# Optimization experiments

Measured on AMD Instinct MI355X. Metric: run time of the kernel, lower is better.

Reference implementation:

```python
import jax, jax.numpy as jnp
import numpy as np

PADDED = 128  # params.get_padded_size()


def setup_inputs() -> dict:
    key = jax.random.key(0)
    k1, k2 = jax.random.split(key)
    B, N, C = 128, 64, 16  # batch, patch size, gridsize**2 channels
    patches = jax.random.normal(k1, (B, N, N, C), dtype=jnp.float32)
    # fractional pixel offsets; keep patches inside the padded canvas
    positions = jax.random.uniform(k2, (B, C, 2), dtype=jnp.float32,
                                   minval=-20.0, maxval=20.0)
    return {"patches": patches, "positions": positions}


def reference(patches, positions):
    """Reassemble overlapping patches into a padded canvas.

    patches:   [B, N, N, C] real patch stack (C = gridsize**2)
    positions: [B, C, 2] per-patch (dy, dx) pixel offsets
    returns:   [B, PADDED, PADDED, 1] sum of translated patches
    """
    B, N, _, C = patches.shape
    M = PADDED
    pad = (M - N) // 2
    # channel -> flat: [B*C, N, N]
    flat = jnp.transpose(patches, (0, 3, 1, 2)).reshape(B * C, N, N)
    # center-pad each patch to the full canvas: [B*C, M, M]
    padded = jnp.pad(flat, ((0, 0), (pad, M - N - pad), (pad, M - N - pad)))
    # Fourier-shift translate by per-patch subpixel offsets
    off = positions.reshape(B * C, 2)
    dy = off[:, 0][:, None, None]
    dx = off[:, 1][:, None, None]
    f = jnp.fft.fftfreq(M).astype(jnp.float32)
    phase = jnp.exp((-2j * jnp.pi) * (f[None, :, None] * dy + f[None, None, :] * dx)).astype(jnp.complex64)
    shifted = jnp.real(jnp.fft.ifft2(jnp.fft.fft2(padded) * phase))
    # flat -> channel, then accumulate (scatter-add) across the C patches
    out = shifted.reshape(B, C, M, M).sum(axis=1)[..., None]
    return out
```

## Files before the change

kernel.cpp:

```cpp
#include <hip/hip_runtime.h>


#define NCH 16
#define CG  4
#define WPB 4

typedef __attribute__((ext_vector_type(8))) short bf16x8;
typedef __attribute__((ext_vector_type(4))) float f32x4;

__device__ __forceinline__ ushort f2bf(float x) {
    union { float f; uint u; } v; v.f = x;
    uint r = v.u + 0x7fffu + ((v.u >> 16) & 1u);
    return (ushort)(r >> 16);
}
__device__ __forceinline__ float bf2f(ushort h) {
    union { uint u; float f; } v; v.u = ((uint)h) << 16; return v.f;
}
__device__ __forceinline__ int uSw(int x) { return (x ^ (x >> 3)) & 7; }

template<bool USE_WS>
__global__ __launch_bounds__(256, 2)
void reassemble_mfma(const float* __restrict__ patches,
                     const float* __restrict__ positions,
                     float* __restrict__ dst, int B)
{
    __shared__ __align__(16) ushort sTab[2][2][8][200];
    __shared__ __align__(16) ushort sP[2][4096];
    __shared__ __align__(16) ushort sU[2][8192];
    __shared__ float sQ[4];

    const int tid  = threadIdx.x;
    const int lane = tid & 63;
    const int wv   = tid >> 6;
    const int nn   = lane & 15;
    const int hh   = lane >> 4;

    int b, cg;
    if (B == 128) {
        const int xcd = blockIdx.x & 7, slot = blockIdx.x >> 3;
        b = xcd * 16 + (slot >> 2); cg = slot & 3;
    } else { b = blockIdx.x >> 2; cg = blockIdx.x & 3; }

    const f32x4 zero = {0.f, 0.f, 0.f, 0.f};
    f32x4 acc[2][8];
    #pragma unroll
    for (int i = 0; i < 2; ++i)
        #pragma unroll
        for (int j = 0; j < 8; ++j) acc[i][j] = zero;
    float Stot = 0.f;

    const float PI = 3.14159265358979323846f;

    for (int cc = 0; cc < CG; ++cc) {
        const int c = cg * CG + cc;
        __syncthreads();

        const float dy = positions[(b * NCH + c) * 2 + 0];
        const float dx = positions[(b * NCH + c) * 2 + 1];
        float kdxf = rintf(dx), kdyf = rintf(dy);
        float sx = sinf((dx - kdxf) * PI); if (((int)kdxf) & 1) sx = -sx;
        float sy = sinf((dy - kdyf) * PI); if (((int)kdyf) & 1) sy = -sy;

        for (int job = tid; job < 384; job += 256) {
            const int tbl = (job >= 192) ? 1 : 0;
            const int j   = job - 192 * tbl;
            const float d  = tbl ? dy : dx;
            const float sd = tbl ? sy : sx;
            const int t = 223 - j;
            float u   = (float)t - d;
            float ur  = u - 128.f * rintf(u * (1.f / 128.f));
            float th  = ur * (PI / 128.f);
            float sth = sinf(th), cth = cosf(th);
            float v = (fabsf(sth) < 1e-12f) ? ((t & 1) ? 128.f : -128.f)
                                            : sd * cth / sth;
            const ushort hi = f2bf(v);
            const ushort lo = f2bf(v - bf2f(hi));
            #pragma unroll
            for (int a = 0; a < 8; ++a) {
                sTab[tbl][0][a][j + a] = hi;
                sTab[tbl][1][a][j + a] = lo;
            }
        }

        float qp = 0.f;
        {
            const float* src = patches + (size_t)b * 65536 + c;
            const int m0 = 2 * (lane & 31);
            const int rb = lane >> 5;
            #pragma unroll
            for (int pp = 0; pp < 8; ++pp) {
                const int r = 16 * wv + 2 * pp + rb;
                const float v0 = src[(size_t)(r * 64 + m0) * 16];
                const float v1 = src[(size_t)(r * 64 + m0 + 1) * 16];
                const int odd = (r + m0) & 1;
                const float s0 = odd ? -v0 : v0;
                const float s1 = odd ? v1 : -v1;
                qp += s0 + s1;
                const ushort h0 = f2bf(s0), h1 = f2bf(s1);
                const ushort l0 = f2bf(s0 - bf2f(h0)), l1 = f2bf(s1 - bf2f(h1));
                const int idx = r * 64 + (((m0 >> 3) ^ (r & 7)) << 3) + (m0 & 7);
                *(uint*)&sP[0][idx] = (uint)h0 | ((uint)h1 << 16);
                *(uint*)&sP[1][idx] = (uint)l0 | ((uint)l1 << 16);
            }
        }
        #pragma unroll
        for (int off = 32; off >= 1; off >>= 1) qp += __shfl_down(qp, off, 64);
        if (lane == 0) sQ[wv] = qp;

        __syncthreads();

        Stot += sx * sy * (sQ[0] + sQ[1] + sQ[2] + sQ[3]);

        f32x4 accA[8];
        #pragma unroll
        for (int tx = 0; tx < 8; ++tx) accA[tx] = zero;

        #pragma unroll
        for (int ks = 0; ks < 2; ++ks) {
            const int r  = 16 * wv + nn;
            const int mc = 4 * ks + hh;
            const bf16x8 Ah = *(const bf16x8*)&sP[0][r * 64 + ((mc ^ (r & 7)) << 3)];
            const bf16x8 Al = *(const bf16x8*)&sP[1][r * 64 + ((mc ^ (r & 7)) << 3)];
            #pragma unroll
            for (int tx = 0; tx < 8; ++tx) {
                const int e0 = 16 * tx + nn + 96 - 32 * ks - 8 * hh;
                const int j0 = 223 - e0;
                const int a  = (-j0) & 7;
                const bf16x8 Bh = *(const bf16x8*)&sTab[0][0][a][j0 + a];
                const bf16x8 Bl = *(const bf16x8*)&sTab[0][1][a][j0 + a];
                accA[tx] = __builtin_amdgcn_mfma_f32_16x16x32_bf16(Ah, Bh, accA[tx], 0, 0, 0);
                accA[tx] = __builtin_amdgcn_mfma_f32_16x16x32_bf16(Ah, Bl, accA[tx], 0, 0, 0);
                accA[tx] = __builtin_amdgcn_mfma_f32_16x16x32_bf16(Al, Bh, accA[tx], 0, 0, 0);
            }
        }

        #pragma unroll
        for (int tx = 0; tx < 8; ++tx) {
            const int x  = 16 * tx + nn;
            const int r0 = 16 * wv + 4 * hh;
            #pragma unroll
            for (int p = 0; p < 2; ++p) {
                const float v0 = accA[tx][2 * p], v1 = accA[tx][2 * p + 1];
                const ushort h0 = f2bf(v0), h1 = f2bf(v1);
                const ushort l0 = f2bf(v0 - bf2f(h0)), l1 = f2bf(v1 - bf2f(h1));
                const int rr  = r0 + 2 * p;
                const int idx = x * 64 + ((((rr >> 3) ^ uSw(x))) << 3) + (rr & 7);
                *(uint*)&sU[0][idx] = (uint)h0 | ((uint)h1 << 16);
                *(uint*)&sU[1][idx] = (uint)l0 | ((uint)l1 << 16);
            }
        }

        __syncthreads();

        #pragma unroll
        for (int ks = 0; ks < 2; ++ks) {
            #pragma unroll
            for (int sp = 0; sp < 3; ++sp) {
                const int sa = (sp == 2) ? 1 : 0;
                const int sb = (sp == 1) ? 1 : 0;
                bf16x8 A0, A1;
                {
                    const int e0 = 16 * (2 * wv + 0) + nn + 96 - 32 * ks - 8 * hh;
                    const int j0 = 223 - e0, a = (-j0) & 7;
                    A0 = *(const bf16x8*)&sTab[1][sa][a][j0 + a];
                }
                {
                    const int e0 = 16 * (2 * wv + 1) + nn + 96 - 32 * ks - 8 * hh;
                    const int j0 = 223 - e0, a = (-j0) & 7;
                    A1 = *(const bf16x8*)&sTab[1][sa][a][j0 + a];
                }
                const int rc = 4 * ks + hh;
                #pragma unroll
                for (int tx = 0; tx < 8; ++tx) {
                    const int x = 16 * tx + nn;
                    const bf16x8 Bu = *(const bf16x8*)&sU[sb][x * 64 + ((rc ^ uSw(x)) << 3)];
                    acc[0][tx] = __builtin_amdgcn_mfma_f32_16x16x32_bf16(A0, Bu, acc[0][tx], 0, 0, 0);
                    acc[1][tx] = __builtin_amdgcn_mfma_f32_16x16x32_bf16(A1, Bu, acc[1][tx], 0, 0, 0);
                }
            }
        }
    }

    const float inv = 1.f / 16384.f;
    if (USE_WS) {
        float* pb = dst + (size_t)(b * WPB + cg) * 16384;
        #pragma unroll
        for (int tyl = 0; tyl < 2; ++tyl)
            #pragma unroll
            for (int g = 0; g < 4; ++g) {
                const int y = 16 * (2 * wv + tyl) + 4 * hh + g;
                #pragma unroll
                for (int tx = 0; tx < 8; ++tx) {
                    const int x = 16 * tx + nn;
                    const float v = (acc[tyl][tx][g] - Stot) * inv;
                    pb[y * 128 + x] = ((x + y) & 1) ? -v : v;
                }
            }
    } else {
        float* ob = dst + (size_t)b * 16384;
        #pragma unroll
        for (int tyl = 0; tyl < 2; ++tyl)
            #pragma unroll
            for (int g = 0; g < 4; ++g) {
                const int y = 16 * (2 * wv + tyl) + 4 * hh + g;
                #pragma unroll
                for (int tx = 0; tx < 8; ++tx) {
                    const int x = 16 * tx + nn;
                    const float v = (acc[tyl][tx][g] - Stot) * inv;
                    atomicAdd(&ob[y * 128 + x], ((x + y) & 1) ? -v : v);
                }
            }
    }
}

__global__ __launch_bounds__(256)
void reduce_kernel(const float* __restrict__ ws, float* __restrict__ out, int B)
{
    const int t4 = blockIdx.x * 256 + threadIdx.x;
    if (t4 >= B * 4096) return;
    const int b = t4 >> 12, q = t4 & 4095;
    const f32x4* w4 = (const f32x4*)ws;
    f32x4 s = w4[(size_t)(b * WPB) * 4096 + q];
    #pragma unroll
    for (int g = 1; g < WPB; ++g) {
        f32x4 v = w4[(size_t)(b * WPB + g) * 4096 + q];
        s[0] += v[0]; s[1] += v[1]; s[2] += v[2]; s[3] += v[3];
    }
    ((f32x4*)out)[t4] = s;
}

extern "C" void kernel_launch(void* const* d_in, const int* in_sizes, int n_in,
                              void* d_out, int out_size, void* d_ws, size_t ws_size,
                              hipStream_t stream)
{
    const float* patches   = (const float*)d_in[0];
    const float* positions = (const float*)d_in[1];
    float* out = (float*)d_out;

    const int B = in_sizes[1] / (NCH * 2);
    const size_t need = (size_t)B * WPB * 16384 * sizeof(float);

    if (ws_size >= need) {
        reassemble_mfma<true><<<dim3(B * 4), dim3(256), 0, stream>>>(
            patches, positions, (float*)d_ws, B);
        reduce_kernel<<<dim3((B * 4096 + 255) / 256), dim3(256), 0, stream>>>(
            (const float*)d_ws, out, B);
    } else {
        hipMemsetAsync(d_out, 0, (size_t)out_size * sizeof(float), stream);
        reassemble_mfma<false><<<dim3(B * 4), dim3(256), 0, stream>>>(
            patches, positions, out, B);
    }
}
```

Measured before the change: 110.1 us.

## Split channels across more blocks and load patch fragments directly into registers

Halves the channels per block (CG 4→2) so the grid doubles to B*8 blocks, with a larger workspace and more partial sums for the reduce kernel. Patch data now goes straight from global memory into MFMA A-fragment registers, which removes the sP shared buffer and one round trip through LDS. The sU stores are widened to 8-byte vector writes, the second-stage loop is reordered to share loads, and the occupancy hint is raised to 3 blocks per CU. The extra workspace traffic in the reduce step and the uncoalesced strided per-lane global loads could offset these savings.

```diff
diff --git a/kernel.cpp b/kernel.cpp
--- a/kernel.cpp
+++ b/kernel.cpp
@@ -2,11 +2,12 @@
 
 
 #define NCH 16
-#define CG  4
-#define WPB 4
+#define CG  2
+#define WPB 8
 
 typedef __attribute__((ext_vector_type(8))) short bf16x8;
 typedef __attribute__((ext_vector_type(4))) float f32x4;
+typedef __attribute__((ext_vector_type(2))) uint uint2v;
 
 __device__ __forceinline__ ushort f2bf(float x) {
     union { float f; uint u; } v; v.f = x;
@@ -19,13 +20,12 @@
 __device__ __forceinline__ int uSw(int x) { return (x ^ (x >> 3)) & 7; }
 
 template<bool USE_WS>
-__global__ __launch_bounds__(256, 2)
+__global__ __launch_bounds__(256, 3)
 void reassemble_mfma(const float* __restrict__ patches,
                      const float* __restrict__ positions,
                      float* __restrict__ dst, int B)
 {
     __shared__ __align__(16) ushort sTab[2][2][8][200];
-    __shared__ __align__(16) ushort sP[2][4096];
     __shared__ __align__(16) ushort sU[2][8192];
     __shared__ float sQ[4];
 
@@ -38,8 +38,8 @@
     int b, cg;
     if (B == 128) {
         const int xcd = blockIdx.x & 7, slot = blockIdx.x >> 3;
-        b = xcd * 16 + (slot >> 2); cg = slot & 3;
-    } else { b = blockIdx.x >> 2; cg = blockIdx.x & 3; }
+        b = xcd * 16 + (slot >> 3); cg = slot & 7;
+    } else { b = blockIdx.x >> 3; cg = blockIdx.x & 7; }
 
     const f32x4 zero = {0.f, 0.f, 0.f, 0.f};
     f32x4 acc[2][8];
@@ -82,25 +82,24 @@
             }
         }
 
+        bf16x8 Ah[2], Al[2];
         float qp = 0.f;
         {
             const float* src = patches + (size_t)b * 65536 + c;
-            const int m0 = 2 * (lane & 31);
-            const int rb = lane >> 5;
-            #pragma unroll
-            for (int pp = 0; pp < 8; ++pp) {
-                const int r = 16 * wv + 2 * pp + rb;
-                const float v0 = src[(size_t)(r * 64 + m0) * 16];
-                const float v1 = src[(size_t)(r * 64 + m0 + 1) * 16];
-                const int odd = (r + m0) & 1;
-                const float s0 = odd ? -v0 : v0;
-                const float s1 = odd ? v1 : -v1;
-                qp += s0 + s1;
-                const ushort h0 = f2bf(s0), h1 = f2bf(s1);
-                const ushort l0 = f2bf(s0 - bf2f(h0)), l1 = f2bf(s1 - bf2f(h1));
-                const int idx = r * 64 + (((m0 >> 3) ^ (r & 7)) << 3) + (m0 & 7);
-                *(uint*)&sP[0][idx] = (uint)h0 | ((uint)h1 << 16);
-                *(uint*)&sP[1][idx] = (uint)l0 | ((uint)l1 << 16);
+            const int r = 16 * wv + nn;
+            #pragma unroll
+            for (int ks = 0; ks < 2; ++ks) {
+                #pragma unroll
+                for (int d8 = 0; d8 < 8; ++d8) {
+                    const int m = 32 * ks + 8 * hh + d8;
+                    const float v  = src[(size_t)(r * 64 + m) * 16];
+                    const float sv = ((r + m) & 1) ? -v : v;
+                    qp += sv;
+                    const ushort h = f2bf(sv);
+                    const ushort l = f2bf(sv - bf2f(h));
+                    Ah[ks][d8] = (short)h;
+                    Al[ks][d8] = (short)l;
+                }
             }
         }
         #pragma unroll
@@ -117,10 +116,6 @@
 
         #pragma unroll
         for (int ks = 0; ks < 2; ++ks) {
-            const int r  = 16 * wv + nn;
-            const int mc = 4 * ks + hh;
-            const bf16x8 Ah = *(const bf16x8*)&sP[0][r * 64 + ((mc ^ (r & 7)) << 3)];
-            const bf16x8 Al = *(const bf16x8*)&sP[1][r * 64 + ((mc ^ (r & 7)) << 3)];
             #pragma unroll
             for (int tx = 0; tx < 8; ++tx) {
                 const int e0 = 16 * tx + nn + 96 - 32 * ks - 8 * hh;
@@ -128,25 +123,29 @@
                 const int a  = (-j0) & 7;
                 const bf16x8 Bh = *(const bf16x8*)&sTab[0][0][a][j0 + a];
                 const bf16x8 Bl = *(const bf16x8*)&sTab[0][1][a][j0 + a];
-                accA[tx] = __builtin_amdgcn_mfma_f32_16x16x32_bf16(Ah, Bh, accA[tx], 0, 0, 0);
-                accA[tx] = __builtin_amdgcn_mfma_f32_16x16x32_bf16(Ah, Bl, accA[tx], 0, 0, 0);
-                accA[tx] = __builtin_amdgcn_mfma_f32_16x16x32_bf16(Al, Bh, accA[tx], 0, 0, 0);
-            }
-        }
-
-        #pragma unroll
-        for (int tx = 0; tx < 8; ++tx) {
-            const int x  = 16 * tx + nn;
+                accA[tx] = __builtin_amdgcn_mfma_f32_16x16x32_bf16(Ah[ks], Bh, accA[tx], 0, 0, 0);
+                accA[tx] = __builtin_amdgcn_mfma_f32_16x16x32_bf16(Ah[ks], Bl, accA[tx], 0, 0, 0);
+                accA[tx] = __builtin_amdgcn_mfma_f32_16x16x32_bf16(Al[ks], Bh, accA[tx], 0, 0, 0);
+            }
+        }
+
+        {
             const int r0 = 16 * wv + 4 * hh;
             #pragma unroll
-            for (int p = 0; p < 2; ++p) {
-                const float v0 = accA[tx][2 * p], v1 = accA[tx][2 * p + 1];
-                const ushort h0 = f2bf(v0), h1 = f2bf(v1);
-                const ushort l0 = f2bf(v0 - bf2f(h0)), l1 = f2bf(v1 - bf2f(h1));
-                const int rr  = r0 + 2 * p;
-                const int idx = x * 64 + ((((rr >> 3) ^ uSw(x))) << 3) + (rr & 7);
-                *(uint*)&sU[0][idx] = (uint)h0 | ((uint)h1 << 16);
-                *(uint*)&sU[1][idx] = (uint)l0 | ((uint)l1 << 16);
+            for (int tx = 0; tx < 8; ++tx) {
+                const int x = 16 * tx + nn;
+                ushort h[4], l[4];
+                #pragma unroll
+                for (int g = 0; g < 4; ++g) {
+                    h[g] = f2bf(accA[tx][g]);
+                    l[g] = f2bf(accA[tx][g] - bf2f(h[g]));
+                }
+                const int idx = x * 64 + ((((r0 >> 3) ^ uSw(x))) << 3) + (r0 & 7);
+                uint2v H, L;
+                H[0] = (uint)h[0] | ((uint)h[1] << 16); H[1] = (uint)h[2] | ((uint)h[3] << 16);
+                L[0] = (uint)l[0] | ((uint)l[1] << 16); L[1] = (uint)l[2] | ((uint)l[3] << 16);
+                *(uint2v*)&sU[0][idx] = H;
+                *(uint2v*)&sU[1][idx] = L;
             }
         }
 
@@ -154,29 +153,32 @@
 
         #pragma unroll
         for (int ks = 0; ks < 2; ++ks) {
-            #pragma unroll
-            for (int sp = 0; sp < 3; ++sp) {
-                const int sa = (sp == 2) ? 1 : 0;
-                const int sb = (sp == 1) ? 1 : 0;
-                bf16x8 A0, A1;
-                {
-                    const int e0 = 16 * (2 * wv + 0) + nn + 96 - 32 * ks - 8 * hh;
-                    const int j0 = 223 - e0, a = (-j0) & 7;
-                    A0 = *(const bf16x8*)&sTab[1][sa][a][j0 + a];
-                }
-                {
-                    const int e0 = 16 * (2 * wv + 1) + nn + 96 - 32 * ks - 8 * hh;
-                    const int j0 = 223 - e0, a = (-j0) & 7;
-                    A1 = *(const bf16x8*)&sTab[1][sa][a][j0 + a];
-                }
-                const int rc = 4 * ks + hh;
-                #pragma unroll
-                for (int tx = 0; tx < 8; ++tx) {
-                    const int x = 16 * tx + nn;
-                    const bf16x8 Bu = *(const bf16x8*)&sU[sb][x * 64 + ((rc ^ uSw(x)) << 3)];
-                    acc[0][tx] = __builtin_amdgcn_mfma_f32_16x16x32_bf16(A0, Bu, acc[0][tx], 0, 0, 0);
-                    acc[1][tx] = __builtin_amdgcn_mfma_f32_16x16x32_bf16(A1, Bu, acc[1][tx], 0, 0, 0);
-                }
+            bf16x8 A0h, A1h, A0l, A1l;
+            {
+                const int e0 = 16 * (2 * wv + 0) + nn + 96 - 32 * ks - 8 * hh;
+                const int j0 = 223 - e0, a = (-j0) & 7;
+                A0h = *(const bf16x8*)&sTab[1][0][a][j0 + a];
+                A0l = *(const bf16x8*)&sTab[1][1][a][j0 + a];
+            }
+            {
+                const int e0 = 16 * (2 * wv + 1) + nn + 96 - 32 * ks - 8 * hh;
+                const int j0 = 223 - e0, a = (-j0) & 7;
+                A1h = *(const bf16x8*)&sTab[1][0][a][j0 + a];
+                A1l = *(const bf16x8*)&sTab[1][1][a][j0 + a];
+            }
+            const int rc = 4 * ks + hh;
+            #pragma unroll
+            for (int tx = 0; tx < 8; ++tx) {
+                const int x = 16 * tx + nn;
+                const int base = x * 64 + ((rc ^ uSw(x)) << 3);
+                const bf16x8 Bu0 = *(const bf16x8*)&sU[0][base];
+                const bf16x8 Bu1 = *(const bf16x8*)&sU[1][base];
+                acc[0][tx] = __builtin_amdgcn_mfma_f32_16x16x32_bf16(A0h, Bu0, acc[0][tx], 0, 0, 0);
+                acc[1][tx] = __builtin_amdgcn_mfma_f32_16x16x32_bf16(A1h, Bu0, acc[1][tx], 0, 0, 0);
+                acc[0][tx] = __builtin_amdgcn_mfma_f32_16x16x32_bf16(A0h, Bu1, acc[0][tx], 0, 0, 0);
+                acc[1][tx] = __builtin_amdgcn_mfma_f32_16x16x32_bf16(A1h, Bu1, acc[1][tx], 0, 0, 0);
+                acc[0][tx] = __builtin_amdgcn_mfma_f32_16x16x32_bf16(A0l, Bu0, acc[0][tx], 0, 0, 0);
+                acc[1][tx] = __builtin_amdgcn_mfma_f32_16x16x32_bf16(A1l, Bu0, acc[1][tx], 0, 0, 0);
             }
         }
     }
@@ -241,13 +243,13 @@
     const size_t need = (size_t)B * WPB * 16384 * sizeof(float);
 
     if (ws_size >= need) {
-        reassemble_mfma<true><<<dim3(B * 4), dim3(256), 0, stream>>>(
+        reassemble_mfma<true><<<dim3(B * WPB), dim3(256), 0, stream>>>(
             patches, positions, (float*)d_ws, B);
         reduce_kernel<<<dim3((B * 4096 + 255) / 256), dim3(256), 0, stream>>>(
             (const float*)d_ws, out, B);
     } else {
         hipMemsetAsync(d_out, 0, (size_t)out_size * sizeof(float), stream);
-        reassemble_mfma<false><<<dim3(B * 4), dim3(256), 0, stream>>>(
+        reassemble_mfma<false><<<dim3(B * WPB), dim3(256), 0, stream>>>(
             patches, positions, out, B);
     }
 }
```

Measured after the change: 178.7 us. +62.3%, slower.
